# Performance work log

Hardware: AMD Instinct MI355X
Metric: run time of the kernel (lower is better)

## Reference

```python
import jax, jax.numpy as jnp
import numpy as np

N_HEAD = 16
NEG = -10000.0


def setup_inputs() -> dict:
    key = jax.random.key(0)
    k1, k2, k3 = jax.random.split(key, 3)
    B, S, NX = 2, 2048, 1024
    x = jax.random.normal(k1, (B, S, NX), dtype=jnp.float32)
    # Conv1D weights: y = x @ W + b (HF Conv1D stores weight as [in, out])
    w_attn = jax.random.normal(k2, (NX, 3 * NX), dtype=jnp.float32) * 0.02
    b_attn = jnp.zeros((3 * NX,), dtype=jnp.float32)
    w_proj = jax.random.normal(k3, (NX, NX), dtype=jnp.float32) * 0.02
    b_proj = jnp.zeros((NX,), dtype=jnp.float32)
    return {"x": x, "w_attn": w_attn, "b_attn": b_attn,
            "w_proj": w_proj, "b_proj": b_proj}


def reference(x, w_attn, b_attn, w_proj, b_proj):
    B, S, NX = x.shape
    H = N_HEAD
    D = NX // H  # head dim
    qkv = x @ w_attn + b_attn                      # [B, S, 3*NX]
    q, k, v = jnp.split(qkv, 3, axis=-1)
    # split heads -> [B, H, S, D]
    q = q.reshape(B, S, H, D).transpose(0, 2, 1, 3)
    k = k.reshape(B, S, H, D).transpose(0, 2, 1, 3)
    v = v.reshape(B, S, H, D).transpose(0, 2, 1, 3)
    # scores [B, H, S, S], scaled (scale=True)
    w = jnp.einsum('bhqd,bhkd->bhqk', q, k) / jnp.sqrt(jnp.asarray(D, x.dtype))
    # causal additive mask exactly as the torch code: w*b + NEG*(1-b)
    bias = jnp.tril(jnp.ones((S, S), dtype=x.dtype))[None, None]  # [1,1,S,S]
    w = w * bias + NEG * (1.0 - bias)
    w = jax.nn.softmax(w, axis=-1)
    a = jnp.einsum('bhqk,bhkd->bhqd', w, v)        # [B, H, S, D]
    a = a.transpose(0, 2, 1, 3).reshape(B, S, NX)  # merge heads
    return a @ w_proj + b_proj
```

## Files before the change

kernel.cpp:

```cpp
#include <hip/hip_runtime.h>
#include <cstdint>
#include <cstddef>


typedef __bf16 bf16;
typedef __bf16 bf16x8 __attribute__((ext_vector_type(8)));
typedef __bf16 bf16x4 __attribute__((ext_vector_type(4)));
typedef float f32x4 __attribute__((ext_vector_type(4)));

#define MFMA16(a, b, c) __builtin_amdgcn_mfma_f32_16x16x32_bf16(a, b, c, 0, 0, 0)

typedef const __attribute__((address_space(1))) void* gas_ptr;
typedef __attribute__((address_space(3))) void* las_ptr;
__device__ __forceinline__ void async16(const void* g, void* l) {
    __builtin_amdgcn_global_load_lds((gas_ptr)g, (las_ptr)l, 16, 0, 0);
}
__device__ __forceinline__ float exp2f_fast(float x) { return __builtin_amdgcn_exp2f(x); }

__global__ __launch_bounds__(256) void prep_kernel(const float* __restrict__ x, bf16* __restrict__ xb,
                                                   const float* __restrict__ wa, bf16* __restrict__ wTa,
                                                   const float* __restrict__ wp, bf16* __restrict__ wTp) {
    __shared__ float tile[32][33];
    const int bid = blockIdx.x, tid = threadIdx.x;
    if (bid < 4096) {
        int i = (bid * 256 + tid) * 4;
        float4 v = *reinterpret_cast<const float4*>(x + i);
        bf16x4 o;
        o[0] = (bf16)v.x; o[1] = (bf16)v.y; o[2] = (bf16)v.z; o[3] = (bf16)v.w;
        *reinterpret_cast<bf16x4*>(xb + i) = o;
        return;
    }
    const float* in; bf16* out; int N, t;
    if (bid < 7168) { t = bid - 4096; in = wa; out = wTa; N = 3072; }
    else            { t = bid - 7168; in = wp; out = wTp; N = 1024; }
    const int K = 1024;
    int bx = t % (N >> 5), by = t / (N >> 5);
    int n0 = bx * 32, k0 = by * 32, tx = tid & 31, ty = tid >> 5;
#pragma unroll
    for (int i = 0; i < 32; i += 8)
        tile[ty + i][tx] = in[(size_t)(k0 + ty + i) * N + n0 + tx];
    __syncthreads();
#pragma unroll
    for (int i = 0; i < 32; i += 8)
        out[(size_t)(n0 + ty + i) * K + k0 + tx] = (bf16)tile[tx][ty + i];
}

template <int OUT_BF16>
__global__ __launch_bounds__(256) void gemm_kernel(const bf16* __restrict__ A,
                                                   const bf16* __restrict__ Bt,
                                                   const float* __restrict__ bias,
                                                   void* __restrict__ Cout,
                                                   int M, int N, int K) {
    __shared__ bf16 Alds[2][128 * 32];
    __shared__ bf16 Blds[2][128 * 32];
    const int tid = threadIdx.x;
    const int w = tid >> 6, l = tid & 63;
    const int lane16 = l & 15, quad = l >> 4;
    const int wr = w >> 1, wc = w & 1;

    const int nwg = gridDim.x * gridDim.y;
    const int lin = blockIdx.x + gridDim.x * blockIdx.y;
    const int q8 = nwg >> 3;
    const int swz = (lin & 7) * q8 + (lin >> 3);
    const int bx = swz % gridDim.x, by = swz / gridDim.x;
    const int row0 = by * 128, col0 = bx * 128;

    const int e = tid * 8;
    const int sr = e >> 5, sc = e & 31;

    f32x4 zero4 = {0.f, 0.f, 0.f, 0.f};
    f32x4 acc[4][4];
#pragma unroll
    for (int i = 0; i < 4; ++i)
#pragma unroll
        for (int j = 0; j < 4; ++j) acc[i][j] = zero4;

#pragma unroll
    for (int ch = 0; ch < 2; ++ch) {
        async16(A + (size_t)(row0 + ch * 64 + sr) * K + sc, &Alds[0][ch * 2048 + e]);
        async16(Bt + (size_t)(col0 + ch * 64 + sr) * K + sc, &Blds[0][ch * 2048 + e]);
    }

    const int niter = K >> 5;
    for (int it = 0; it < niter; ++it) {
        const int cur = it & 1;
        __syncthreads();
        if (it + 1 < niter) {
            const int k1 = (it + 1) << 5;
#pragma unroll
            for (int ch = 0; ch < 2; ++ch) {
                async16(A + (size_t)(row0 + ch * 64 + sr) * K + k1 + sc, &Alds[cur ^ 1][ch * 2048 + e]);
                async16(Bt + (size_t)(col0 + ch * 64 + sr) * K + k1 + sc, &Blds[cur ^ 1][ch * 2048 + e]);
            }
        }
        bf16x8 af[4], bfr[4];
#pragma unroll
        for (int i = 0; i < 4; ++i) {
            af[i] = *reinterpret_cast<const bf16x8*>(&Alds[cur][(64 * wr + 16 * i + lane16) * 32 + quad * 8]);
            bfr[i] = *reinterpret_cast<const bf16x8*>(&Blds[cur][(64 * wc + 16 * i + lane16) * 32 + quad * 8]);
        }
#pragma unroll
        for (int i = 0; i < 4; ++i)
#pragma unroll
            for (int j = 0; j < 4; ++j) acc[i][j] = MFMA16(af[i], bfr[j], acc[i][j]);
    }

#pragma unroll
    for (int i = 0; i < 4; ++i)
#pragma unroll
        for (int j = 0; j < 4; ++j)
#pragma unroll
            for (int r = 0; r < 4; ++r) {
                int row = row0 + 64 * wr + 16 * i + quad * 4 + r;
                int col = col0 + 64 * wc + 16 * j + lane16;
                float v = acc[i][j][r] + bias[col];
                if (OUT_BF16)
                    reinterpret_cast<bf16*>(Cout)[(size_t)row * N + col] = (bf16)v;
                else
                    reinterpret_cast<float*>(Cout)[(size_t)row * N + col] = v;
            }
}

template <int OUT_BF16>
__global__ __launch_bounds__(256) void gemm64k_kernel(const bf16* __restrict__ A,
                                                      const bf16* __restrict__ Bt,
                                                      const float* __restrict__ bias,
                                                      void* __restrict__ Cout,
                                                      int M, int N, int K) {
    __shared__ bf16 Alds[2][64 * 64];
    __shared__ bf16 Blds[2][128 * 64];
    const int tid = threadIdx.x;
    const int w = tid >> 6, l = tid & 63;
    const int lane16 = l & 15, quad = l >> 4;
    const int wr = w >> 1, wc = w & 1;
    const int row0 = blockIdx.y * 64, col0 = blockIdx.x * 128;

    f32x4 zero4 = {0.f, 0.f, 0.f, 0.f};
    f32x4 acc[2][4];
#pragma unroll
    for (int i = 0; i < 2; ++i)
#pragma unroll
        for (int j = 0; j < 4; ++j) acc[i][j] = zero4;

    auto stage = [&](int buf, int k0) {
#pragma unroll
        for (int c = 0; c < 2; ++c) {
            int idx = c * 256 + tid;
            int r = idx >> 3, cc = idx & 7, gc = cc ^ (r & 7);
            async16(A + (size_t)(row0 + r) * K + k0 + gc * 8, &Alds[buf][idx * 8]);
        }
#pragma unroll
        for (int c = 0; c < 4; ++c) {
            int idx = c * 256 + tid;
            int r = idx >> 3, cc = idx & 7, gc = cc ^ (r & 7);
            async16(Bt + (size_t)(col0 + r) * K + k0 + gc * 8, &Blds[buf][idx * 8]);
        }
    };

    stage(0, 0);
    const int niter = K >> 6;
    for (int it = 0; it < niter; ++it) {
        const int cur = it & 1;
        __syncthreads();
        if (it + 1 < niter) stage(cur ^ 1, (it + 1) << 6);
        bf16x8 af[2][2], bfr[4][2];
#pragma unroll
        for (int i = 0; i < 2; ++i) {
            int r = 32 * wr + 16 * i + lane16;
#pragma unroll
            for (int ks = 0; ks < 2; ++ks) {
                int cc = (quad + 4 * ks) ^ (r & 7);
                af[i][ks] = *reinterpret_cast<const bf16x8*>(&Alds[cur][r * 64 + cc * 8]);
            }
        }
#pragma unroll
        for (int j = 0; j < 4; ++j) {
            int r = 64 * wc + 16 * j + lane16;
#pragma unroll
            for (int ks = 0; ks < 2; ++ks) {
                int cc = (quad + 4 * ks) ^ (r & 7);
                bfr[j][ks] = *reinterpret_cast<const bf16x8*>(&Blds[cur][r * 64 + cc * 8]);
            }
        }
#pragma unroll
        for (int ks = 0; ks < 2; ++ks)
#pragma unroll
            for (int i = 0; i < 2; ++i)
#pragma unroll
                for (int j = 0; j < 4; ++j) acc[i][j] = MFMA16(af[i][ks], bfr[j][ks], acc[i][j]);
    }

#pragma unroll
    for (int i = 0; i < 2; ++i)
#pragma unroll
        for (int j = 0; j < 4; ++j)
#pragma unroll
            for (int r = 0; r < 4; ++r) {
                int row = row0 + 32 * wr + 16 * i + quad * 4 + r;
                int col = col0 + 64 * wc + 16 * j + lane16;
                float v = acc[i][j][r] + bias[col];
                if (OUT_BF16)
                    reinterpret_cast<bf16*>(Cout)[(size_t)row * N + col] = (bf16)v;
                else
                    reinterpret_cast<float*>(Cout)[(size_t)row * N + col] = v;
            }
}

__global__ __launch_bounds__(256) void attn_kernel(const bf16* __restrict__ qkv,
                                                   bf16* __restrict__ aout) {
    const int S = 2048;
    const int bh = blockIdx.x;
    const int b = bh >> 4, hd = bh & 15;
    const int rr = blockIdx.y >> 3, j = blockIdx.y & 7;
    const int qt = (rr == 0) ? (31 - j) : (rr == 1) ? (16 + j) : (rr == 2) ? (15 - j) : j;
    const int nkt = qt + 1;
    const int tid = threadIdx.x, w = tid >> 6, l = tid & 63;
    const int lane16 = l & 15, quad = l >> 4;

    __shared__ bf16 Klds[2][64 * 64];
    __shared__ bf16 Vt[2][64 * 64];
    __shared__ bf16 Plds[4][16 * 64];

    const bf16* base = qkv + (size_t)b * S * 3072;
    const float qscale = 0.125f * 1.4426950408889634f;
    const float NEGs = -10000.0f * 1.4426950408889634f;

    bf16x8 qf[2];
#pragma unroll
    for (int hv = 0; hv < 2; ++hv) {
        const bf16* qp = base + (size_t)(qt * 64 + 16 * w + lane16) * 3072 + hd * 64;
        bf16x8 t = *reinterpret_cast<const bf16x8*>(qp + hv * 32 + quad * 8);
#pragma unroll
        for (int jj = 0; jj < 8; ++jj) t[jj] = (bf16)((float)t[jj] * qscale);
        qf[hv] = t;
    }

    f32x4 zero4 = {0.f, 0.f, 0.f, 0.f};
    f32x4 o[4];
#pragma unroll
    for (int df = 0; df < 4; ++df) o[df] = zero4;
    float lsum = 0.f;

    const int kr = tid >> 3, kcc = tid & 7;
    const int vp = tid & 31, vd = (tid >> 5) * 8;
    bf16x8 kreg0, kreg1, vreg0, vreg1;
    auto load_tile = [&](int kt) {
        const bf16* tb = base + (size_t)(kt * 64) * 3072;
        kreg0 = *reinterpret_cast<const bf16x8*>(tb + (size_t)kr * 3072 + 1024 + hd * 64 + kcc * 8);
        kreg1 = *reinterpret_cast<const bf16x8*>(tb + (size_t)(32 + kr) * 3072 + 1024 + hd * 64 + kcc * 8);
        vreg0 = *reinterpret_cast<const bf16x8*>(tb + (size_t)(2 * vp) * 3072 + 2048 + hd * 64 + vd);
        vreg1 = *reinterpret_cast<const bf16x8*>(tb + (size_t)(2 * vp + 1) * 3072 + 2048 + hd * 64 + vd);
    };
    auto write_KV = [&](int buf) {
        bf16* Kb = &Klds[buf][0];
        bf16* Vb = &Vt[buf][0];
        const int kchunk = kcc ^ (kr & 7);
        *reinterpret_cast<bf16x8*>(&Kb[kr * 64 + kchunk * 8]) = kreg0;
        *reinterpret_cast<bf16x8*>(&Kb[(32 + kr) * 64 + kchunk * 8]) = kreg1;
#pragma unroll
        for (int jj = 0; jj < 8; ++jj) {
            int row = vd + jj;
            union { bf16 h2v[2]; uint32_t u; } pk;
            pk.h2v[0] = vreg0[jj]; pk.h2v[1] = vreg1[jj];
            int idx = row * 64 + (((vp >> 2) ^ (row & 7)) * 8) + (vp & 3) * 2;
            *reinterpret_cast<uint32_t*>(&Vb[idx]) = pk.u;
        }
    };

    load_tile(0);
    write_KV(0);
    if (nkt > 1) load_tile(1);
    __syncthreads();

    for (int kt = 0; kt < nkt; ++kt) {
        const int p = kt & 1;
        if (kt + 1 < nkt) write_KV(p ^ 1);

        const bf16* Kb = &Klds[p][0];
        const bf16* Vb = &Vt[p][0];

        __builtin_amdgcn_s_setprio(1);
        f32x4 st[4];
#pragma unroll
        for (int kf = 0; kf < 4; ++kf) {
            int row = kf * 16 + lane16;
            int c0 = quad ^ (row & 7);
            int c1 = (4 + quad) ^ (row & 7);
            bf16x8 k0 = *reinterpret_cast<const bf16x8*>(&Kb[row * 64 + c0 * 8]);
            bf16x8 k1 = *reinterpret_cast<const bf16x8*>(&Kb[row * 64 + c1 * 8]);
            f32x4 z = zero4;
            z = MFMA16(k0, qf[0], z);
            z = MFMA16(k1, qf[1], z);
            st[kf] = z;
        }
        __builtin_amdgcn_s_setprio(0);

        if (kt + 2 < nkt) load_tile(kt + 2);

        if (kt == qt) {
            const int q = qt * 64 + 16 * w + lane16;
#pragma unroll
            for (int kf = 0; kf < 4; ++kf)
#pragma unroll
                for (int r = 0; r < 4; ++r)
                    if (kt * 64 + kf * 16 + quad * 4 + r > q) st[kf][r] = NEGs;
        }

        float rs = 0.f;
        bf16* Prow = &Plds[w][lane16 * 64];
        const int rx = lane16 & 7;
#pragma unroll
        for (int kf = 0; kf < 4; ++kf) {
            bf16x4 pk;
#pragma unroll
            for (int r = 0; r < 4; ++r) {
                float pv = exp2f_fast(st[kf][r]);
                rs += pv;
                pk[r] = (bf16)pv;
            }
            int chunk = (2 * kf + (quad >> 1)) ^ rx;
            *reinterpret_cast<bf16x4*>(Prow + chunk * 8 + (quad & 1) * 4) = pk;
        }
        lsum += rs;

        __builtin_amdgcn_s_setprio(1);
#pragma unroll
        for (int kf2 = 0; kf2 < 2; ++kf2) {
            int pc = (kf2 * 4 + quad) ^ rx;
            bf16x8 pf = *reinterpret_cast<const bf16x8*>(&Plds[w][lane16 * 64 + pc * 8]);
#pragma unroll
            for (int df = 0; df < 4; ++df) {
                int vrow = df * 16 + lane16;
                int vc = (kf2 * 4 + quad) ^ (vrow & 7);
                bf16x8 vf = *reinterpret_cast<const bf16x8*>(&Vb[vrow * 64 + vc * 8]);
                o[df] = MFMA16(pf, vf, o[df]);
            }
        }
        __builtin_amdgcn_s_setprio(0);

        __syncthreads();
    }

    lsum += __shfl_xor(lsum, 16, 64);
    lsum += __shfl_xor(lsum, 32, 64);
    float inv = 1.0f / lsum;

#pragma unroll
    for (int r = 0; r < 4; ++r) {
        float li = __shfl(inv, quad * 4 + r, 64);
        int row = qt * 64 + 16 * w + quad * 4 + r;
#pragma unroll
        for (int df = 0; df < 4; ++df)
            aout[(size_t)(b * S + row) * 1024 + hd * 64 + df * 16 + lane16] =
                (bf16)(o[df][r] * li);
    }
}

extern "C" void kernel_launch(void* const* d_in, const int* in_sizes, int n_in,
                              void* d_out, int out_size, void* d_ws, size_t ws_size,
                              hipStream_t stream) {
    const float* x      = (const float*)d_in[0];
    const float* w_attn = (const float*)d_in[1];
    const float* b_attn = (const float*)d_in[2];
    const float* w_proj = (const float*)d_in[3];
    const float* b_proj = (const float*)d_in[4];
    float* out = (float*)d_out;
    char* ws = (char*)d_ws;

    const int Mtok = 4096, NX = 1024, N3 = 3072;
    bf16* xb   = (bf16*)(ws);
    bf16* wTa  = (bf16*)(ws + ((size_t)8 << 20));
    bf16* wTp  = (bf16*)(ws + ((size_t)14 << 20));
    bf16* qkv  = (bf16*)(ws + ((size_t)16 << 20));
    bf16* abuf = (bf16*)(ws + ((size_t)40 << 20));

    prep_kernel<<<dim3(8192), 256, 0, stream>>>(x, xb, w_attn, wTa, w_proj, wTp);
    gemm_kernel<1><<<dim3(N3 / 128, Mtok / 128), 256, 0, stream>>>(xb, wTa, b_attn, qkv, Mtok, N3, NX);
    attn_kernel<<<dim3(32, 32), 256, 0, stream>>>(qkv, abuf);
    gemm64k_kernel<0><<<dim3(NX / 128, Mtok / 64), 256, 0, stream>>>(abuf, wTp, b_proj, out, Mtok, NX, NX);
}
```

Measured before the change: 169.3 us.

## Swizzle LDS layout in QKV GEMM and use 64x64 tiles for output projection

The QKV GEMM's LDS staging now uses an XOR-swizzled layout that packs two 32-wide K rows into one 64-element row, so the fragment reads avoid bank conflicts. The output projection GEMM switches from 64x128 tiles to 64x64 tiles, launching 1024 workgroups instead of 512 for better CU occupancy, and adds grouped block-index swizzling for L2 reuse. Smaller tiles raise the global load traffic per FLOP and lower MFMA work per wave.

```diff
diff --git a/kernel.cpp b/kernel.cpp
--- a/kernel.cpp
+++ b/kernel.cpp
@@ -65,8 +65,15 @@
     const int bx = swz % gridDim.x, by = swz / gridDim.x;
     const int row0 = by * 128, col0 = bx * 128;
 
-    const int e = tid * 8;
-    const int sr = e >> 5, sc = e & 31;
+    int grs[2], gks[2];
+#pragma unroll
+    for (int c = 0; c < 2; ++c) {
+        int idx = c * 256 + tid;
+        int R = idx >> 3, pos = idx & 7;
+        int pos2 = pos ^ (R & 7);
+        grs[c] = 2 * R + (pos2 >> 2);
+        gks[c] = (pos2 & 3) * 8;
+    }
 
     f32x4 zero4 = {0.f, 0.f, 0.f, 0.f};
     f32x4 acc[4][4];
@@ -75,29 +82,32 @@
 #pragma unroll
         for (int j = 0; j < 4; ++j) acc[i][j] = zero4;
 
-#pragma unroll
-    for (int ch = 0; ch < 2; ++ch) {
-        async16(A + (size_t)(row0 + ch * 64 + sr) * K + sc, &Alds[0][ch * 2048 + e]);
-        async16(Bt + (size_t)(col0 + ch * 64 + sr) * K + sc, &Blds[0][ch * 2048 + e]);
-    }
-
+    auto stage = [&](int buf, int k0) {
+#pragma unroll
+        for (int c = 0; c < 2; ++c) {
+            int idx = c * 256 + tid;
+            async16(A + (size_t)(row0 + grs[c]) * K + k0 + gks[c], &Alds[buf][idx * 8]);
+            async16(Bt + (size_t)(col0 + grs[c]) * K + k0 + gks[c], &Blds[buf][idx * 8]);
+        }
+    };
+
+    stage(0, 0);
     const int niter = K >> 5;
     for (int it = 0; it < niter; ++it) {
         const int cur = it & 1;
         __syncthreads();
-        if (it + 1 < niter) {
-            const int k1 = (it + 1) << 5;
-#pragma unroll
-            for (int ch = 0; ch < 2; ++ch) {
-                async16(A + (size_t)(row0 + ch * 64 + sr) * K + k1 + sc, &Alds[cur ^ 1][ch * 2048 + e]);
-                async16(Bt + (size_t)(col0 + ch * 64 + sr) * K + k1 + sc, &Blds[cur ^ 1][ch * 2048 + e]);
-            }
-        }
+        if (it + 1 < niter) stage(cur ^ 1, (it + 1) << 5);
         bf16x8 af[4], bfr[4];
 #pragma unroll
         for (int i = 0; i < 4; ++i) {
-            af[i] = *reinterpret_cast<const bf16x8*>(&Alds[cur][(64 * wr + 16 * i + lane16) * 32 + quad * 8]);
-            bfr[i] = *reinterpret_cast<const bf16x8*>(&Blds[cur][(64 * wc + 16 * i + lane16) * 32 + quad * 8]);
+            int gra = 64 * wr + 16 * i + lane16;
+            int Ra = gra >> 1;
+            int pa = ((gra & 1) * 4 + quad) ^ (Ra & 7);
+            af[i] = *reinterpret_cast<const bf16x8*>(&Alds[cur][Ra * 64 + pa * 8]);
+            int grb = 64 * wc + 16 * i + lane16;
+            int Rb = grb >> 1;
+            int pb = ((grb & 1) * 4 + quad) ^ (Rb & 7);
+            bfr[i] = *reinterpret_cast<const bf16x8*>(&Blds[cur][Rb * 64 + pb * 8]);
         }
 #pragma unroll
         for (int i = 0; i < 4; ++i)
@@ -121,26 +131,31 @@
             }
 }
 
-template <int OUT_BF16>
-__global__ __launch_bounds__(256) void gemm64k_kernel(const bf16* __restrict__ A,
-                                                      const bf16* __restrict__ Bt,
-                                                      const float* __restrict__ bias,
-                                                      void* __restrict__ Cout,
-                                                      int M, int N, int K) {
+__global__ __launch_bounds__(256) void gemm64sq_kernel(const bf16* __restrict__ A,
+                                                       const bf16* __restrict__ Bt,
+                                                       const float* __restrict__ bias,
+                                                       float* __restrict__ Cout,
+                                                       int M, int N, int K) {
     __shared__ bf16 Alds[2][64 * 64];
-    __shared__ bf16 Blds[2][128 * 64];
+    __shared__ bf16 Blds[2][64 * 64];
     const int tid = threadIdx.x;
     const int w = tid >> 6, l = tid & 63;
     const int lane16 = l & 15, quad = l >> 4;
     const int wr = w >> 1, wc = w & 1;
-    const int row0 = blockIdx.y * 64, col0 = blockIdx.x * 128;
+
+    const int nwg = gridDim.x * gridDim.y;
+    const int lin = blockIdx.x + gridDim.x * blockIdx.y;
+    const int q8 = nwg >> 3;
+    const int swz = (lin & 7) * q8 + (lin >> 3);
+    const int bx = swz % gridDim.x, by = swz / gridDim.x;
+    const int row0 = by * 64, col0 = bx * 64;
 
     f32x4 zero4 = {0.f, 0.f, 0.f, 0.f};
-    f32x4 acc[2][4];
+    f32x4 acc[2][2];
 #pragma unroll
     for (int i = 0; i < 2; ++i)
 #pragma unroll
-        for (int j = 0; j < 4; ++j) acc[i][j] = zero4;
+        for (int j = 0; j < 2; ++j) acc[i][j] = zero4;
 
     auto stage = [&](int buf, int k0) {
 #pragma unroll
@@ -148,11 +163,6 @@
             int idx = c * 256 + tid;
             int r = idx >> 3, cc = idx & 7, gc = cc ^ (r & 7);
             async16(A + (size_t)(row0 + r) * K + k0 + gc * 8, &Alds[buf][idx * 8]);
-        }
-#pragma unroll
-        for (int c = 0; c < 4; ++c) {
-            int idx = c * 256 + tid;
-            int r = idx >> 3, cc = idx & 7, gc = cc ^ (r & 7);
             async16(Bt + (size_t)(col0 + r) * K + k0 + gc * 8, &Blds[buf][idx * 8]);
         }
     };
@@ -163,7 +173,7 @@
         const int cur = it & 1;
         __syncthreads();
         if (it + 1 < niter) stage(cur ^ 1, (it + 1) << 6);
-        bf16x8 af[2][2], bfr[4][2];
+        bf16x8 af[2][2], bfr[2][2];
 #pragma unroll
         for (int i = 0; i < 2; ++i) {
             int r = 32 * wr + 16 * i + lane16;
@@ -174,8 +184,8 @@
             }
         }
 #pragma unroll
-        for (int j = 0; j < 4; ++j) {
-            int r = 64 * wc + 16 * j + lane16;
+        for (int j = 0; j < 2; ++j) {
+            int r = 32 * wc + 16 * j + lane16;
 #pragma unroll
             for (int ks = 0; ks < 2; ++ks) {
                 int cc = (quad + 4 * ks) ^ (r & 7);
@@ -187,22 +197,18 @@
 #pragma unroll
             for (int i = 0; i < 2; ++i)
 #pragma unroll
-                for (int j = 0; j < 4; ++j) acc[i][j] = MFMA16(af[i][ks], bfr[j][ks], acc[i][j]);
+                for (int j = 0; j < 2; ++j) acc[i][j] = MFMA16(af[i][ks], bfr[j][ks], acc[i][j]);
     }
 
 #pragma unroll
     for (int i = 0; i < 2; ++i)
 #pragma unroll
-        for (int j = 0; j < 4; ++j)
+        for (int j = 0; j < 2; ++j)
 #pragma unroll
             for (int r = 0; r < 4; ++r) {
                 int row = row0 + 32 * wr + 16 * i + quad * 4 + r;
-                int col = col0 + 64 * wc + 16 * j + lane16;
-                float v = acc[i][j][r] + bias[col];
-                if (OUT_BF16)
-                    reinterpret_cast<bf16*>(Cout)[(size_t)row * N + col] = (bf16)v;
-                else
-                    reinterpret_cast<float*>(Cout)[(size_t)row * N + col] = v;
+                int col = col0 + 32 * wc + 16 * j + lane16;
+                Cout[(size_t)row * N + col] = acc[i][j][r] + bias[col];
             }
 }
 
@@ -377,5 +383,5 @@
     prep_kernel<<<dim3(8192), 256, 0, stream>>>(x, xb, w_attn, wTa, w_proj, wTp);
     gemm_kernel<1><<<dim3(N3 / 128, Mtok / 128), 256, 0, stream>>>(xb, wTa, b_attn, qkv, Mtok, N3, NX);
     attn_kernel<<<dim3(32, 32), 256, 0, stream>>>(qkv, abuf);
-    gemm64k_kernel<0><<<dim3(NX / 128, Mtok / 64), 256, 0, stream>>>(abuf, wTp, b_proj, out, Mtok, NX, NX);
-}
+    gemm64sq_kernel<<<dim3(NX / 64, Mtok / 64), 256, 0, stream>>>(abuf, wTp, b_proj, out, Mtok, NX, NX);
+}
```

Measured after the change: 169.6 us. Within noise of the previous version (+0.2%).
